# Kernel tuning notes

Measured on AMD Instinct MI355X. Metric: run time of the kernel, lower is better.

Reference implementation:

```python
import jax, jax.numpy as jnp
import numpy as np

# ---- static config (mirrors PointRend init kwargs) ----
H, W = 512, 512          # img_size
CH, CW = 128, 128        # coarse_size
FH, FW = 256, 256        # fine_size
CF = 256                 # fine_channels
NC = 3                   # num_classes (forced by MLP's hard-coded 259/131 channel counts)
NPTS = 2048              # N points
K_OVER = 3               # k oversampling
BELTA = 0.75
NUM_OVER = K_OVER * NPTS          # 6144
STEP1 = int(NPTS * BELTA)         # 1536 uncertain points
STEP2 = NPTS - STEP1              # 512 coverage points


def _xavier(key, c_out, c_in):
    std = (2.0 / (c_in + c_out)) ** 0.5
    return jax.random.normal(key, (c_out, c_in), jnp.float32) * std


def setup_inputs() -> dict:
    key = jax.random.key(0)
    k1, k2, k3, k4, k5, k6 = jax.random.split(key, 6)
    fine_grained = jax.random.normal(k1, (2, CF, FH, FW), jnp.float32)
    coarse_pre = jax.random.normal(k2, (2, NC, CH, CW), jnp.float32)
    # torch.randperm(H*W) done inside forward in the original; passed in for determinism
    random_1d_index = jax.random.permutation(k3, H * W).astype(jnp.int32)
    w1 = _xavier(k4, 256, CF + NC)   # conv1: 1x1, in=259, out=256, no bias
    w2 = _xavier(k5, 128, 256 + 3)   # conv2: in=259, out=128
    w3 = _xavier(k6, NC, 128 + 3)    # conv3: in=131, out=num_classes
    prelu_a = jnp.array(0.25, jnp.float32)  # shared single-param PReLU
    return dict(fine_grained=fine_grained, coarse_pre=coarse_pre,
                w1=w1, w2=w2, w3=w3, prelu_a=prelu_a,
                random_1d_index=random_1d_index)


def _bilinear(x, h, w):
    # matches nn.Upsample(mode='bilinear', align_corners=False)
    return jax.image.resize(x, (x.shape[0], x.shape[1], h, w), method="bilinear")


def _prelu(x, a):
    return jnp.where(x >= 0, x, a * x)


def _mlp(feat, w1, w2, w3, a):
    # feat: [B, N, C] -> channels-first [B, C, N]; BatchNorms in MLP are unused in forward.
    x = jnp.transpose(feat, (0, 2, 1))
    tail = x[:, -3:, :]  # last 3 channels appended to each layer's input
    l1 = _prelu(jnp.einsum('bcn,oc->bon', x, w1), a)
    l2 = _prelu(jnp.einsum('bcn,oc->bon', jnp.concatenate([l1, tail], 1), w2), a)
    return jnp.einsum('bcn,oc->bon', jnp.concatenate([l2, tail], 1), w3)  # [B, NC, N]


def reference(fine_grained, coarse_pre, w1, w2, w3, prelu_a, random_1d_index):
    B = fine_grained.shape[0]
    up_coarse_o = _bilinear(coarse_pre, H, W)            # [B, NC, H, W] logits
    up_coarse_sm = jax.nn.softmax(up_coarse_o, axis=1)   # softmax over classes
    up_fine = _bilinear(fine_grained, H, W)              # [B, CF, H, W]

    h_idx = random_1d_index // W
    w_idx = random_1d_index % W
    all_index = jnp.stack([h_idx, w_idx], axis=1)        # [H*W, 2]
    cand = all_index[:NUM_OVER]                          # oversampled candidates

    # vectorized replacement of the python loop: gather probs at candidates
    over_pre = up_coarse_sm[:, :, cand[:, 0], cand[:, 1]].transpose(0, 2, 1)  # [B, NUM_OVER, NC]
    top2, _ = jax.lax.top_k(over_pre, 2)
    uncertain = 1.0 - (top2[..., 0] - top2[..., 1])      # [B, NUM_OVER]
    _, u_idx = jax.lax.top_k(uncertain, STEP1)           # [B, STEP1]
    u_pts = cand[u_idx]                                  # [B, STEP1, 2]
    cov = jnp.broadcast_to(all_index[-STEP2:][None], (B, STEP2, 2))
    pts = jnp.concatenate([u_pts, cov], axis=1)          # [B, N, 2]

    # masked_select traverses the dense mask in row-major (h,w) order -> sort linear ids
    lin = pts[..., 0] * W + pts[..., 1]                  # [B, N]
    lin_sorted = jnp.sort(lin, axis=1)
    sh, sw = lin_sorted // W, lin_sorted % W
    bidx = jnp.arange(B)[:, None]
    sel_coarse = up_coarse_o[bidx, :, sh, sw]            # [B, N, NC] (pre-softmax feats)
    sel_fine = up_fine[bidx, :, sh, sw]                  # [B, N, CF]

    # faithful to torch: flat concat of the two masked_select outputs, then reshape
    feat = jnp.concatenate([sel_fine.reshape(-1), sel_coarse.reshape(-1)]).reshape(B, NPTS, -1)

    out = _mlp(feat, w1, w2, w3, prelu_a)                # [B, NC, N]
    mask = jnp.zeros((B, H, W), jnp.int32).at[bidx, pts[..., 0], pts[..., 1]].add(1)
    return out, mask
```

## Files before the change

kernel.cpp:

```cpp
#include <hip/hip_runtime.h>
#include <hip/hip_bf16.h>

#define NPTS 2048
#define NOVER 6144
#define STEP1 1536
#define STEP2 512
#define HW_TOT 262144

__device__ __forceinline__ float prelu_f(float x, float a) { return x >= 0.0f ? x : a * x; }

__device__ __forceinline__ void coarse_coords(int h, int w, float& fy, float& fx,
                                              int& y0, int& y1, int& x0, int& x1) {
  float sy = (h + 0.5f) * 0.25f - 0.5f;
  float sx = (w + 0.5f) * 0.25f - 0.5f;
  float yf = floorf(sy), xf = floorf(sx);
  fy = sy - yf; fx = sx - xf;
  int yi = (int)yf, xi = (int)xf;
  y0 = min(127, max(0, yi)); y1 = min(127, max(0, yi + 1));
  x0 = min(127, max(0, xi)); x1 = min(127, max(0, xi + 1));
}

__device__ __forceinline__ float coarse_sample(const float* __restrict__ ch, float fy, float fx,
                                               int y0, int y1, int x0, int x1) {
  float v00 = ch[(y0 << 7) + x0];
  float v01 = ch[(y0 << 7) + x1];
  float v10 = ch[(y1 << 7) + x0];
  float v11 = ch[(y1 << 7) + x1];
  return (1.0f - fy) * ((1.0f - fx) * v00 + fx * v01) + fy * ((1.0f - fx) * v10 + fx * v11);
}

__global__ __launch_bounds__(256) void pr_fill_v5(uint4* __restrict__ p) {
  p[blockIdx.x * 256 + threadIdx.x] = make_uint4(0u, 0u, 0u, 0u);
}

__global__ __launch_bounds__(256) void pr_wprep_v5(const float* __restrict__ w1,
                                                   const float* __restrict__ w2,
                                                   float* __restrict__ wT1,
                                                   float* __restrict__ wT2) {
  int gid = blockIdx.x * 256 + threadIdx.x;
  if (gid < 259 * 256) {
    int c = gid >> 8, o = gid & 255;
    wT1[c * 256 + o] = w1[o * 259 + c];
  } else {
    int g2 = gid - 259 * 256;
    if (g2 < 259 * 128) {
      int c = g2 >> 7, o = g2 & 127;
      wT2[c * 128 + o] = w2[o * 259 + c];
    }
  }
}

__global__ __launch_bounds__(256) void pr_uncert_v5(const float* __restrict__ coarse,
                                                    const int* __restrict__ ridx,
                                                    unsigned* __restrict__ keys) {
  int gid = blockIdx.x * 256 + threadIdx.x;
  if (gid >= 2 * NOVER) return;
  int b = gid / NOVER, i = gid - b * NOVER;
  int lin = ridx[i];
  int h = lin >> 9, w = lin & 511;
  float fy, fx; int y0, y1, x0, x1;
  coarse_coords(h, w, fy, fx, y0, y1, x0, x1);
  const float* cb = coarse + (((size_t)b * 3) << 14);
  float p0 = coarse_sample(cb, fy, fx, y0, y1, x0, x1);
  float p1 = coarse_sample(cb + (1 << 14), fy, fx, y0, y1, x0, x1);
  float p2 = coarse_sample(cb + (2 << 14), fy, fx, y0, y1, x0, x1);
  float m = fmaxf(p0, fmaxf(p1, p2));
  float e0 = expf(p0 - m), e1 = expf(p1 - m), e2 = expf(p2 - m);
  float s = e0 + e1 + e2;
  float q0 = e0 / s, q1 = e1 / s, q2 = e2 / s;
  float a0 = q0, a1 = q1, a2 = q2, tmp;
  if (a0 < a1) { tmp = a0; a0 = a1; a1 = tmp; }
  if (a1 < a2) { tmp = a1; a1 = a2; a2 = tmp; }
  if (a0 < a1) { tmp = a0; a0 = a1; a1 = tmp; }
  float u = 1.0f - (a0 - a1);
  keys[gid] = __float_as_uint(u);
}

__global__ __launch_bounds__(1024) void pr_topk_v5(const unsigned* __restrict__ keys,
                                                   const int* __restrict__ ridx,
                                                   int* __restrict__ lin_sorted,
                                                   float* __restrict__ mask) {
  __shared__ unsigned kv[NOVER];
  __shared__ unsigned bitmap[8192];
  __shared__ unsigned hist[256];
  __shared__ unsigned short tiebuf[NOVER];
  __shared__ unsigned scanbuf[16];
  __shared__ unsigned selinfo[2];
  __shared__ int tiecnt;
  const int b = blockIdx.x, t = threadIdx.x;
  const int lane = t & 63, wid = t >> 6;

  for (int i = t; i < NOVER; i += 1024) kv[i] = keys[b * NOVER + i];
  for (int i = t; i < 8192; i += 1024) bitmap[i] = 0u;
  if (t == 0) { selinfo[1] = STEP1; tiecnt = 0; }
  __syncthreads();

  unsigned prefix = 0u;
  for (int pass = 0; pass < 4; ++pass) {
    const int shift = 24 - 8 * pass;
    const unsigned maskHi = (pass == 0) ? 0u : (0xFFFFFFFFu << (shift + 8));
    for (int i = t; i < 256; i += 1024) hist[i] = 0u;
    __syncthreads();
    for (int i = t; i < NOVER; i += 1024) {
      unsigned k = kv[i];
      if ((k & maskHi) == prefix) atomicAdd(&hist[(k >> shift) & 255u], 1u);
    }
    __syncthreads();
    if (t < 64) {
      unsigned h0 = hist[t * 4], h1 = hist[t * 4 + 1], h2 = hist[t * 4 + 2], h3 = hist[t * 4 + 3];
      unsigned q = h0 + h1 + h2 + h3;
      unsigned s = q;
      for (int off = 1; off < 64; off <<= 1) {
        unsigned n = __shfl_down(s, off);
        if (t + off < 64) s += n;
      }
      unsigned exq = s - q;
      unsigned R = selinfo[1];
      unsigned se3 = exq, se2 = se3 + h3, se1 = se2 + h2, se0 = se1 + h1;
      if (se3 < R && R <= se3 + h3)      { selinfo[0] = prefix | ((unsigned)(t * 4 + 3) << shift); selinfo[1] = R - se3; }
      else if (se2 < R && R <= se2 + h2) { selinfo[0] = prefix | ((unsigned)(t * 4 + 2) << shift); selinfo[1] = R - se2; }
      else if (se1 < R && R <= se1 + h1) { selinfo[0] = prefix | ((unsigned)(t * 4 + 1) << shift); selinfo[1] = R - se1; }
      else if (se0 < R && R <= se0 + h0) { selinfo[0] = prefix | ((unsigned)(t * 4 + 0) << shift); selinfo[1] = R - se0; }
    }
    __syncthreads();
    prefix = selinfo[0];
  }
  const unsigned T = prefix;
  const int r = (int)selinfo[1];

  for (int i = t; i < NOVER; i += 1024) {
    unsigned k = kv[i];
    if (k > T) {
      int lin = ridx[i];
      mask[(size_t)b * HW_TOT + lin] = 1.0f;
      atomicOr(&bitmap[lin >> 5], 1u << (lin & 31));
    } else if (k == T) {
      int pos = atomicAdd(&tiecnt, 1);
      tiebuf[pos] = (unsigned short)i;
    }
  }
  for (int i = t; i < STEP2; i += 1024) {
    int lin = ridx[HW_TOT - STEP2 + i];
    mask[(size_t)b * HW_TOT + lin] = 1.0f;
    atomicOr(&bitmap[lin >> 5], 1u << (lin & 31));
  }
  __syncthreads();
  const int m = tiecnt;
  for (int j = t; j < m; j += 1024) {
    int idx = tiebuf[j];
    int rank = 0;
    for (int jj = 0; jj < m; ++jj) rank += (tiebuf[jj] < idx) ? 1 : 0;
    if (rank < r) {
      int lin = ridx[idx];
      mask[(size_t)b * HW_TOT + lin] = 1.0f;
      atomicOr(&bitmap[lin >> 5], 1u << (lin & 31));
    }
  }
  __syncthreads();

  unsigned mySum = 0;
#pragma unroll
  for (int q = 0; q < 8; ++q) mySum += __popc(bitmap[t * 8 + q]);
  unsigned v = mySum;
  for (int off = 1; off < 64; off <<= 1) {
    unsigned n = __shfl_up(v, off);
    if (lane >= off) v += n;
  }
  if (lane == 63) scanbuf[wid] = v;
  __syncthreads();
  if (t == 0) {
    unsigned run = 0;
    for (int w16 = 0; w16 < 16; ++w16) { unsigned tmp = scanbuf[w16]; scanbuf[w16] = run; run += tmp; }
  }
  __syncthreads();
  unsigned pos = (v - mySum) + scanbuf[wid];
  for (int q = 0; q < 8; ++q) {
    unsigned word = bitmap[t * 8 + q];
    int basebit = (t * 8 + q) << 5;
    while (word) {
      int bit = __ffs(word) - 1;
      word &= word - 1;
      lin_sorted[b * NPTS + pos++] = basebit + bit;
    }
  }
}

__global__ __launch_bounds__(256) void pr_gather_v5(const float* __restrict__ fine,
                                                    const float* __restrict__ coarse,
                                                    const int* __restrict__ lin_sorted,
                                                    float* __restrict__ feat) {
  const int g = blockIdx.x;
  for (int c = threadIdx.x; c < 259; c += 256) {
    int j = g * 259 + c;
    float v;
    if (j < 1048576) {
      int nsrc = j >> 8, ch = j & 255;
      int bs = nsrc >> 11;
      int lin = lin_sorted[nsrc];
      int h = lin >> 9, w = lin & 511;
      float sy = (h + 0.5f) * 0.5f - 0.5f;
      float sx = (w + 0.5f) * 0.5f - 0.5f;
      float yf = floorf(sy), xf = floorf(sx);
      float fy = sy - yf, fx = sx - xf;
      int yi = (int)yf, xi = (int)xf;
      int y0 = min(255, max(0, yi)), y1 = min(255, max(0, yi + 1));
      int x0 = min(255, max(0, xi)), x1 = min(255, max(0, xi + 1));
      const float* base = fine + (((size_t)(bs * 256 + ch)) << 16);
      float v00 = base[(y0 << 8) + x0];
      float v01 = base[(y0 << 8) + x1];
      float v10 = base[(y1 << 8) + x0];
      float v11 = base[(y1 << 8) + x1];
      v = (1.0f - fy) * ((1.0f - fx) * v00 + fx * v01) + fy * ((1.0f - fx) * v10 + fx * v11);
    } else {
      int jj = j - 1048576;
      int nsrc = jj / 3;
      int kk = jj - nsrc * 3;
      int bs = nsrc >> 11;
      int lin = lin_sorted[nsrc];
      int h = lin >> 9, w = lin & 511;
      float fy, fx; int y0, y1, x0, x1;
      coarse_coords(h, w, fy, fx, y0, y1, x0, x1);
      v = coarse_sample(coarse + (((size_t)bs * 3 + kk) << 14), fy, fx, y0, y1, x0, x1);
    }
    feat[j] = v;
  }
}

__global__ __launch_bounds__(256) void pr_mlp_v5(const float* __restrict__ feat,
                                                 const float* __restrict__ wT1,
                                                 const float* __restrict__ wT2,
                                                 const float* __restrict__ w3,
                                                 const float* __restrict__ pa,
                                                 float* __restrict__ out) {
  __shared__ __align__(16) float xs[259][16];
  __shared__ __align__(16) float l1t[256][16];
  __shared__ __align__(16) float l2t[128][16];
  const int t = threadIdx.x;
  const int g0 = blockIdx.x * 16;
  const float a = pa[0];

  const float* fb = feat + g0 * 259;
  for (int i = t; i < 16 * 259; i += 256) {
    int p = i / 259;
    int c = i - p * 259;
    xs[c][p] = fb[i];
  }
  __syncthreads();

  {
    const int ob = (t & 63) * 4;
    const int pb = (t >> 6) * 4;
    float acc[4][4];
#pragma unroll
    for (int i = 0; i < 4; ++i)
#pragma unroll
      for (int q = 0; q < 4; ++q) acc[i][q] = 0.0f;
    for (int c = 0; c < 259; ++c) {
      const float4 wv = *(const float4*)&wT1[c * 256 + ob];
      const float4 xv = *(const float4*)&xs[c][pb];
      acc[0][0] = fmaf(wv.x, xv.x, acc[0][0]); acc[0][1] = fmaf(wv.x, xv.y, acc[0][1]);
      acc[0][2] = fmaf(wv.x, xv.z, acc[0][2]); acc[0][3] = fmaf(wv.x, xv.w, acc[0][3]);
      acc[1][0] = fmaf(wv.y, xv.x, acc[1][0]); acc[1][1] = fmaf(wv.y, xv.y, acc[1][1]);
      acc[1][2] = fmaf(wv.y, xv.z, acc[1][2]); acc[1][3] = fmaf(wv.y, xv.w, acc[1][3]);
      acc[2][0] = fmaf(wv.z, xv.x, acc[2][0]); acc[2][1] = fmaf(wv.z, xv.y, acc[2][1]);
      acc[2][2] = fmaf(wv.z, xv.z, acc[2][2]); acc[2][3] = fmaf(wv.z, xv.w, acc[2][3]);
      acc[3][0] = fmaf(wv.w, xv.x, acc[3][0]); acc[3][1] = fmaf(wv.w, xv.y, acc[3][1]);
      acc[3][2] = fmaf(wv.w, xv.z, acc[3][2]); acc[3][3] = fmaf(wv.w, xv.w, acc[3][3]);
    }
#pragma unroll
    for (int i = 0; i < 4; ++i) {
      l1t[ob + i][pb + 0] = prelu_f(acc[i][0], a);
      l1t[ob + i][pb + 1] = prelu_f(acc[i][1], a);
      l1t[ob + i][pb + 2] = prelu_f(acc[i][2], a);
      l1t[ob + i][pb + 3] = prelu_f(acc[i][3], a);
    }
  }
  __syncthreads();

  {
    const int ob = (t & 31) * 4;
    const int pb = (t >> 5) * 2;
    float acc[4][2];
#pragma unroll
    for (int i = 0; i < 4; ++i) { acc[i][0] = 0.0f; acc[i][1] = 0.0f; }
    for (int c = 0; c < 256; ++c) {
      const float4 wv = *(const float4*)&wT2[c * 128 + ob];
      const float2 xv = *(const float2*)&l1t[c][pb];
      acc[0][0] = fmaf(wv.x, xv.x, acc[0][0]); acc[0][1] = fmaf(wv.x, xv.y, acc[0][1]);
      acc[1][0] = fmaf(wv.y, xv.x, acc[1][0]); acc[1][1] = fmaf(wv.y, xv.y, acc[1][1]);
      acc[2][0] = fmaf(wv.z, xv.x, acc[2][0]); acc[2][1] = fmaf(wv.z, xv.y, acc[2][1]);
      acc[3][0] = fmaf(wv.w, xv.x, acc[3][0]); acc[3][1] = fmaf(wv.w, xv.y, acc[3][1]);
    }
#pragma unroll
    for (int kk = 0; kk < 3; ++kk) {
      const float4 wv = *(const float4*)&wT2[(256 + kk) * 128 + ob];
      const float x0 = xs[256 + kk][pb], x1 = xs[256 + kk][pb + 1];
      acc[0][0] = fmaf(wv.x, x0, acc[0][0]); acc[0][1] = fmaf(wv.x, x1, acc[0][1]);
      acc[1][0] = fmaf(wv.y, x0, acc[1][0]); acc[1][1] = fmaf(wv.y, x1, acc[1][1]);
      acc[2][0] = fmaf(wv.z, x0, acc[2][0]); acc[2][1] = fmaf(wv.z, x1, acc[2][1]);
      acc[3][0] = fmaf(wv.w, x0, acc[3][0]); acc[3][1] = fmaf(wv.w, x1, acc[3][1]);
    }
#pragma unroll
    for (int i = 0; i < 4; ++i) {
      l2t[ob + i][pb + 0] = prelu_f(acc[i][0], a);
      l2t[ob + i][pb + 1] = prelu_f(acc[i][1], a);
    }
  }
  __syncthreads();

  if (t < 48) {
    const int o3 = t % 3, p = t / 3;
    const float* wr = w3 + o3 * 131;
    float s = 0.0f;
    for (int c = 0; c < 128; ++c) s = fmaf(wr[c], l2t[c][p], s);
#pragma unroll
    for (int kk = 0; kk < 3; ++kk) s = fmaf(wr[128 + kk], xs[256 + kk][p], s);
    const int g = g0 + p;
    out[((g >> 11) * 3 + o3) * 2048 + (g & 2047)] = s;
  }
}

extern "C" void kernel_launch(void* const* d_in, const int* in_sizes, int n_in,
                              void* d_out, int out_size, void* d_ws, size_t ws_size,
                              hipStream_t stream) {
  const float* fine   = (const float*)d_in[0];
  const float* coarse = (const float*)d_in[1];
  const float* w1     = (const float*)d_in[2];
  const float* w2     = (const float*)d_in[3];
  const float* w3     = (const float*)d_in[4];
  const float* pa     = (const float*)d_in[5];
  const int*   ridx   = (const int*)d_in[6];

  float* out  = (float*)d_out;
  float* mask = out + 2 * 3 * 2048;

  char* ws = (char*)d_ws;
  int*      lin_sorted = (int*)ws;
  float*    wT1  = (float*)(ws + 16384);
  float*    wT2  = (float*)(ws + 281600);
  unsigned* keys = (unsigned*)(ws + 414208);
  float*    feat = (float*)(ws + 463360);

  pr_fill_v5<<<512, 256, 0, stream>>>((uint4*)mask);
  pr_wprep_v5<<<389, 256, 0, stream>>>(w1, w2, wT1, wT2);
  pr_uncert_v5<<<48, 256, 0, stream>>>(coarse, ridx, keys);
  pr_topk_v5<<<2, 1024, 0, stream>>>(keys, ridx, lin_sorted, mask);
  pr_gather_v5<<<4096, 256, 0, stream>>>(fine, coarse, lin_sorted, feat);
  pr_mlp_v5<<<256, 256, 0, stream>>>(feat, wT1, wT2, w3, pa, out);
}
```

Baseline: 260.8 us.

## Merge prep kernels into one launch and halve MLP points per block

```diff
diff --git a/kernel.cpp b/kernel.cpp
--- a/kernel.cpp
+++ b/kernel.cpp
@@ -29,54 +29,54 @@
   return (1.0f - fy) * ((1.0f - fx) * v00 + fx * v01) + fy * ((1.0f - fx) * v10 + fx * v11);
 }
 
-__global__ __launch_bounds__(256) void pr_fill_v5(uint4* __restrict__ p) {
-  p[blockIdx.x * 256 + threadIdx.x] = make_uint4(0u, 0u, 0u, 0u);
-}
-
-__global__ __launch_bounds__(256) void pr_wprep_v5(const float* __restrict__ w1,
-                                                   const float* __restrict__ w2,
-                                                   float* __restrict__ wT1,
-                                                   float* __restrict__ wT2) {
-  int gid = blockIdx.x * 256 + threadIdx.x;
-  if (gid < 259 * 256) {
-    int c = gid >> 8, o = gid & 255;
-    wT1[c * 256 + o] = w1[o * 259 + c];
+__global__ __launch_bounds__(256) void pr_prep_v6(const float* __restrict__ w1,
+                                                  const float* __restrict__ w2,
+                                                  const float* __restrict__ coarse,
+                                                  const int* __restrict__ ridx,
+                                                  float* __restrict__ wT1,
+                                                  float* __restrict__ wT2,
+                                                  unsigned* __restrict__ keys,
+                                                  uint4* __restrict__ maskv) {
+  const int blk = blockIdx.x, t = threadIdx.x;
+  if (blk < 512) {
+    maskv[blk * 256 + t] = make_uint4(0u, 0u, 0u, 0u);
+  } else if (blk < 901) {
+    int gid = (blk - 512) * 256 + t;
+    if (gid < 259 * 256) {
+      int c = gid >> 8, o = gid & 255;
+      wT1[c * 256 + o] = w1[o * 259 + c];
+    } else {
+      int g2 = gid - 259 * 256;
+      if (g2 < 259 * 128) {
+        int c = g2 >> 7, o = g2 & 127;
+        wT2[c * 128 + o] = w2[o * 259 + c];
+      }
+    }
   } else {
-    int g2 = gid - 259 * 256;
-    if (g2 < 259 * 128) {
-      int c = g2 >> 7, o = g2 & 127;
-      wT2[c * 128 + o] = w2[o * 259 + c];
-    }
-  }
-}
-
-__global__ __launch_bounds__(256) void pr_uncert_v5(const float* __restrict__ coarse,
-                                                    const int* __restrict__ ridx,
-                                                    unsigned* __restrict__ keys) {
-  int gid = blockIdx.x * 256 + threadIdx.x;
-  if (gid >= 2 * NOVER) return;
-  int b = gid / NOVER, i = gid - b * NOVER;
-  int lin = ridx[i];
-  int h = lin >> 9, w = lin & 511;
-  float fy, fx; int y0, y1, x0, x1;
-  coarse_coords(h, w, fy, fx, y0, y1, x0, x1);
-  const float* cb = coarse + (((size_t)b * 3) << 14);
-  float p0 = coarse_sample(cb, fy, fx, y0, y1, x0, x1);
-  float p1 = coarse_sample(cb + (1 << 14), fy, fx, y0, y1, x0, x1);
-  float p2 = coarse_sample(cb + (2 << 14), fy, fx, y0, y1, x0, x1);
-  float m = fmaxf(p0, fmaxf(p1, p2));
-  float e0 = expf(p0 - m), e1 = expf(p1 - m), e2 = expf(p2 - m);
-  float s = e0 + e1 + e2;
-  float q0 = e0 / s, q1 = e1 / s, q2 = e2 / s;
-  float a0 = q0, a1 = q1, a2 = q2, tmp;
-  if (a0 < a1) { tmp = a0; a0 = a1; a1 = tmp; }
-  if (a1 < a2) { tmp = a1; a1 = a2; a2 = tmp; }
-  if (a0 < a1) { tmp = a0; a0 = a1; a1 = tmp; }
-  float u = 1.0f - (a0 - a1);
-  keys[gid] = __float_as_uint(u);
-}
-
-__global__ __launch_bounds__(1024) void pr_topk_v5(const unsigned* __restrict__ keys,
+    int gid = (blk - 901) * 256 + t;
+    int b = gid / NOVER, i = gid - b * NOVER;
+    int lin = ridx[i];
+    int h = lin >> 9, w = lin & 511;
+    float fy, fx; int y0, y1, x0, x1;
+    coarse_coords(h, w, fy, fx, y0, y1, x0, x1);
+    const float* cb = coarse + (((size_t)b * 3) << 14);
+    float p0 = coarse_sample(cb, fy, fx, y0, y1, x0, x1);
+    float p1 = coarse_sample(cb + (1 << 14), fy, fx, y0, y1, x0, x1);
+    float p2 = coarse_sample(cb + (2 << 14), fy, fx, y0, y1, x0, x1);
+    float m = fmaxf(p0, fmaxf(p1, p2));
+    float e0 = expf(p0 - m), e1 = expf(p1 - m), e2 = expf(p2 - m);
+    float s = e0 + e1 + e2;
+    float q0 = e0 / s, q1 = e1 / s, q2 = e2 / s;
+    float a0 = q0, a1 = q1, a2 = q2, tmp;
+    if (a0 < a1) { tmp = a0; a0 = a1; a1 = tmp; }
+    if (a1 < a2) { tmp = a1; a1 = a2; a2 = tmp; }
+    if (a0 < a1) { tmp = a0; a0 = a1; a1 = tmp; }
+    float u = 1.0f - (a0 - a1);
+    keys[gid] = __float_as_uint(u);
+  }
+}
+
+__global__ __launch_bounds__(1024) void pr_topk_v6(const unsigned* __restrict__ keys,
                                                    const int* __restrict__ ridx,
                                                    int* __restrict__ lin_sorted,
                                                    float* __restrict__ mask) {
@@ -185,7 +185,7 @@
   }
 }
 
-__global__ __launch_bounds__(256) void pr_gather_v5(const float* __restrict__ fine,
+__global__ __launch_bounds__(256) void pr_gather_v6(const float* __restrict__ fine,
                                                     const float* __restrict__ coarse,
                                                     const int* __restrict__ lin_sorted,
                                                     float* __restrict__ feat) {
@@ -226,95 +226,90 @@
   }
 }
 
-__global__ __launch_bounds__(256) void pr_mlp_v5(const float* __restrict__ feat,
+__global__ __launch_bounds__(256) void pr_mlp_v6(const float* __restrict__ feat,
                                                  const float* __restrict__ wT1,
                                                  const float* __restrict__ wT2,
                                                  const float* __restrict__ w3,
                                                  const float* __restrict__ pa,
                                                  float* __restrict__ out) {
-  __shared__ __align__(16) float xs[259][16];
-  __shared__ __align__(16) float l1t[256][16];
-  __shared__ __align__(16) float l2t[128][16];
+  __shared__ __align__(16) float xsf[8 * 259];
+  __shared__ __align__(16) float l1[8 * 256];
+  __shared__ __align__(16) float l2[8 * 128];
   const int t = threadIdx.x;
-  const int g0 = blockIdx.x * 16;
+  const int g0 = blockIdx.x * 8;
   const float a = pa[0];
 
-  const float* fb = feat + g0 * 259;
-  for (int i = t; i < 16 * 259; i += 256) {
-    int p = i / 259;
-    int c = i - p * 259;
-    xs[c][p] = fb[i];
+  {
+    const float4* src = (const float4*)(feat + g0 * 259);
+    float4* dst = (float4*)xsf;
+    for (int i = t; i < 518; i += 256) dst[i] = src[i];
   }
   __syncthreads();
 
   {
     const int ob = (t & 63) * 4;
-    const int pb = (t >> 6) * 4;
-    float acc[4][4];
-#pragma unroll
-    for (int i = 0; i < 4; ++i)
-#pragma unroll
-      for (int q = 0; q < 4; ++q) acc[i][q] = 0.0f;
+    const int pb = (t >> 6) * 2;
+    float acc[4][2];
+#pragma unroll
+    for (int i = 0; i < 4; ++i) { acc[i][0] = 0.0f; acc[i][1] = 0.0f; }
+    const float* x0p = xsf + pb * 259;
+    const float* x1p = xsf + (pb + 1) * 259;
     for (int c = 0; c < 259; ++c) {
       const float4 wv = *(const float4*)&wT1[c * 256 + ob];
-      const float4 xv = *(const float4*)&xs[c][pb];
-      acc[0][0] = fmaf(wv.x, xv.x, acc[0][0]); acc[0][1] = fmaf(wv.x, xv.y, acc[0][1]);
-      acc[0][2] = fmaf(wv.x, xv.z, acc[0][2]); acc[0][3] = fmaf(wv.x, xv.w, acc[0][3]);
-      acc[1][0] = fmaf(wv.y, xv.x, acc[1][0]); acc[1][1] = fmaf(wv.y, xv.y, acc[1][1]);
-      acc[1][2] = fmaf(wv.y, xv.z, acc[1][2]); acc[1][3] = fmaf(wv.y, xv.w, acc[1][3]);
-      acc[2][0] = fmaf(wv.z, xv.x, acc[2][0]); acc[2][1] = fmaf(wv.z, xv.y, acc[2][1]);
-      acc[2][2] = fmaf(wv.z, xv.z, acc[2][2]); acc[2][3] = fmaf(wv.z, xv.w, acc[2][3]);
-      acc[3][0] = fmaf(wv.w, xv.x, acc[3][0]); acc[3][1] = fmaf(wv.w, xv.y, acc[3][1]);
-      acc[3][2] = fmaf(wv.w, xv.z, acc[3][2]); acc[3][3] = fmaf(wv.w, xv.w, acc[3][3]);
-    }
-#pragma unroll
-    for (int i = 0; i < 4; ++i) {
-      l1t[ob + i][pb + 0] = prelu_f(acc[i][0], a);
-      l1t[ob + i][pb + 1] = prelu_f(acc[i][1], a);
-      l1t[ob + i][pb + 2] = prelu_f(acc[i][2], a);
-      l1t[ob + i][pb + 3] = prelu_f(acc[i][3], a);
+      const float xv0 = x0p[c];
+      const float xv1 = x1p[c];
+      acc[0][0] = fmaf(wv.x, xv0, acc[0][0]); acc[0][1] = fmaf(wv.x, xv1, acc[0][1]);
+      acc[1][0] = fmaf(wv.y, xv0, acc[1][0]); acc[1][1] = fmaf(wv.y, xv1, acc[1][1]);
+      acc[2][0] = fmaf(wv.z, xv0, acc[2][0]); acc[2][1] = fmaf(wv.z, xv1, acc[2][1]);
+      acc[3][0] = fmaf(wv.w, xv0, acc[3][0]); acc[3][1] = fmaf(wv.w, xv1, acc[3][1]);
+    }
+#pragma unroll
+    for (int q = 0; q < 2; ++q) {
+      float4 r;
+      r.x = prelu_f(acc[0][q], a); r.y = prelu_f(acc[1][q], a);
+      r.z = prelu_f(acc[2][q], a); r.w = prelu_f(acc[3][q], a);
+      *(float4*)&l1[(pb + q) * 256 + ob] = r;
     }
   }
   __syncthreads();
 
   {
     const int ob = (t & 31) * 4;
-    const int pb = (t >> 5) * 2;
-    float acc[4][2];
-#pragma unroll
-    for (int i = 0; i < 4; ++i) { acc[i][0] = 0.0f; acc[i][1] = 0.0f; }
+    const int p = t >> 5;
+    float acc[4] = {0.0f, 0.0f, 0.0f, 0.0f};
+    const float* xp = l1 + p * 256;
     for (int c = 0; c < 256; ++c) {
       const float4 wv = *(const float4*)&wT2[c * 128 + ob];
-      const float2 xv = *(const float2*)&l1t[c][pb];
-      acc[0][0] = fmaf(wv.x, xv.x, acc[0][0]); acc[0][1] = fmaf(wv.x, xv.y, acc[0][1]);
-      acc[1][0] = fmaf(wv.y, xv.x, acc[1][0]); acc[1][1] = fmaf(wv.y, xv.y, acc[1][1]);
-      acc[2][0] = fmaf(wv.z, xv.x, acc[2][0]); acc[2][1] = fmaf(wv.z, xv.y, acc[2][1]);
-      acc[3][0] = fmaf(wv.w, xv.x, acc[3][0]); acc[3][1] = fmaf(wv.w, xv.y, acc[3][1]);
+      const float xv = xp[c];
+      acc[0] = fmaf(wv.x, xv, acc[0]);
+      acc[1] = fmaf(wv.y, xv, acc[1]);
+      acc[2] = fmaf(wv.z, xv, acc[2]);
+      acc[3] = fmaf(wv.w, xv, acc[3]);
     }
 #pragma unroll
     for (int kk = 0; kk < 3; ++kk) {
       const float4 wv = *(const float4*)&wT2[(256 + kk) * 128 + ob];
-      const float x0 = xs[256 + kk][pb], x1 = xs[256 + kk][pb + 1];
-      acc[0][0] = fmaf(wv.x, x0, acc[0][0]); acc[0][1] = fmaf(wv.x, x1, acc[0][1]);
-      acc[1][0] = fmaf(wv.y, x0, acc[1][0]); acc[1][1] = fmaf(wv.y, x1, acc[1][1]);
-      acc[2][0] = fmaf(wv.z, x0, acc[2][0]); acc[2][1] = fmaf(wv.z, x1, acc[2][1]);
-      acc[3][0] = fmaf(wv.w, x0, acc[3][0]); acc[3][1] = fmaf(wv.w, x1, acc[3][1]);
-    }
-#pragma unroll
-    for (int i = 0; i < 4; ++i) {
-      l2t[ob + i][pb + 0] = prelu_f(acc[i][0], a);
-      l2t[ob + i][pb + 1] = prelu_f(acc[i][1], a);
-    }
-  }
-  __syncthreads();
-
-  if (t < 48) {
+      const float xv = xsf[p * 259 + 256 + kk];
+      acc[0] = fmaf(wv.x, xv, acc[0]);
+      acc[1] = fmaf(wv.y, xv, acc[1]);
+      acc[2] = fmaf(wv.z, xv, acc[2]);
+      acc[3] = fmaf(wv.w, xv, acc[3]);
+    }
+    float4 r;
+    r.x = prelu_f(acc[0], a); r.y = prelu_f(acc[1], a);
+    r.z = prelu_f(acc[2], a); r.w = prelu_f(acc[3], a);
+    *(float4*)&l2[p * 128 + ob] = r;
+  }
+  __syncthreads();
+
+  if (t < 24) {
     const int o3 = t % 3, p = t / 3;
     const float* wr = w3 + o3 * 131;
+    const float* xp = l2 + p * 128;
     float s = 0.0f;
-    for (int c = 0; c < 128; ++c) s = fmaf(wr[c], l2t[c][p], s);
-#pragma unroll
-    for (int kk = 0; kk < 3; ++kk) s = fmaf(wr[128 + kk], xs[256 + kk][p], s);
+    for (int c = 0; c < 128; ++c) s = fmaf(wr[c], xp[c], s);
+#pragma unroll
+    for (int kk = 0; kk < 3; ++kk) s = fmaf(wr[128 + kk], xsf[p * 259 + 256 + kk], s);
     const int g = g0 + p;
     out[((g >> 11) * 3 + o3) * 2048 + (g & 2047)] = s;
   }
@@ -341,10 +336,8 @@
   unsigned* keys = (unsigned*)(ws + 414208);
   float*    feat = (float*)(ws + 463360);
 
-  pr_fill_v5<<<512, 256, 0, stream>>>((uint4*)mask);
-  pr_wprep_v5<<<389, 256, 0, stream>>>(w1, w2, wT1, wT2);
-  pr_uncert_v5<<<48, 256, 0, stream>>>(coarse, ridx, keys);
-  pr_topk_v5<<<2, 1024, 0, stream>>>(keys, ridx, lin_sorted, mask);
-  pr_gather_v5<<<4096, 256, 0, stream>>>(fine, coarse, lin_sorted, feat);
-  pr_mlp_v5<<<256, 256, 0, stream>>>(feat, wT1, wT2, w3, pa, out);
-}
+  pr_prep_v6<<<949, 256, 0, stream>>>(w1, w2, coarse, ridx, wT1, wT2, keys, (uint4*)mask);
+  pr_topk_v6<<<2, 1024, 0, stream>>>(keys, ridx, lin_sorted, mask);
+  pr_gather_v6<<<4096, 256, 0, stream>>>(fine, coarse, lin_sorted, feat);
+  pr_mlp_v6<<<512, 256, 0, stream>>>(feat, wT1, wT2, w3, pa, out);
+}
```

Result: no change. 259.1 us (-0.6%).
